# Kernel tuning notes

Measured on AMD Instinct MI355X. Metric: run time of the kernel, lower is better.

## Reference

```python
import jax, jax.numpy as jnp
import numpy as np

E = 1024  # embed_dim

def setup_inputs() -> dict:
    key = jax.random.key(0)
    ks = jax.random.split(key, 7)
    s = 1.0 / np.sqrt(E)  # torch Linear default init scale (uniform bound)
    x = jax.random.normal(ks[0], (4, 2048, E), dtype=jnp.float32)
    Wq = jax.random.uniform(ks[1], (E, E), jnp.float32, -s, s)
    bq = jax.random.uniform(ks[2], (E,), jnp.float32, -s, s)
    Wk = jax.random.uniform(ks[3], (E, E), jnp.float32, -s, s)
    bk = jax.random.uniform(ks[4], (E,), jnp.float32, -s, s)
    Wv = jax.random.uniform(ks[5], (E, E), jnp.float32, -s, s)
    bv = jax.random.uniform(ks[6], (E,), jnp.float32, -s, s)
    return {"x": x, "Wq": Wq, "bq": bq, "Wk": Wk, "bk": bk, "Wv": Wv, "bv": bv}

def reference(x, Wq, bq, Wk, bk, Wv, bv):
    # torch nn.Linear: y = x @ W.T + b
    Q = jnp.einsum('bse,fe->bsf', x, Wq) + bq
    K = jnp.einsum('bse,fe->bsf', x, Wk) + bk
    V = jnp.einsum('bse,fe->bsf', x, Wv) + bv
    scale = jnp.sqrt(jnp.asarray(E, x.dtype))
    scores = jnp.einsum('bqd,bkd->bqk', Q, K) / scale  # [B,S,S]
    attn = jax.nn.softmax(scores, axis=-1)
    return jnp.einsum('bqk,bkd->bqd', attn, V)
```

## Files before the change

### kernel.cpp

```cpp
#include <hip/hip_runtime.h>
#include <hip/hip_bf16.h>


typedef __attribute__((ext_vector_type(8))) short bf16x8;
typedef __attribute__((ext_vector_type(4))) float f32x4;

#define DEVI static __device__ __forceinline__

DEVI short to_bf16(float f) {
    unsigned u = __builtin_bit_cast(unsigned, f);
    u += 0x7fffu + ((u >> 16) & 1u);
    return (short)(u >> 16);
}
DEVI float from_bf16(short s) {
    return __builtin_bit_cast(float, (unsigned)((unsigned short)s) << 16);
}

DEVI void gload_lds16(const short* g, short* l) {
    __builtin_amdgcn_global_load_lds(
        (const __attribute__((address_space(1))) void*)g,
        (__attribute__((address_space(3))) void*)l, 16, 0, 0);
}

template<int BIAS, typename TOUT>
__global__ __launch_bounds__(256, 3)
void gemm97(const short* __restrict__ A, long lda, long bsA,
            const short* __restrict__ B, long ldb, long bsB,
            const float* __restrict__ b0, const float* __restrict__ b1,
            const float* __restrict__ b2,
            TOUT* __restrict__ c0, TOUT* __restrict__ c1, TOUT* __restrict__ c2,
            long ldc, long bsC, int K, float scale)
{
    __shared__ __align__(16) short As[128 * 64];
    __shared__ __align__(16) short Bs[128 * 64];

    const int tid = threadIdx.x;
    const int z = blockIdx.z;

    const int gx = gridDim.x;
    const int nwg = gx * gridDim.y;
    const int id = blockIdx.y * gx + blockIdx.x;
    const int id2 = (id & 7) * (nwg >> 3) + (id >> 3);
    const long m0 = (long)(id2 / gx) * 128;
    const long n0 = (long)(id2 % gx) * 128;

    const short* Ab = A + (long)z * bsA + m0 * lda;
    const short* Bb = B + (long)z * bsB + n0 * ldb;

    const int wv = tid >> 6;
    const int lane = tid & 63;
    const int wr = (wv >> 1) * 64;
    const int wc = (wv & 1) * 64;
    const int lrow = lane & 15;
    const int q = lane >> 4;

    const int NT = K >> 6;

    auto stage = [&](int t) {
        const long k0 = (long)t * 64;
        #pragma unroll
        for (int i = 0; i < 4; ++i) {
            int s = i * 256 + tid;
            int row = s >> 3;
            int src = (s & 7) ^ (row & 7);
            gload_lds16(Ab + (long)row * lda + k0 + src * 8, &As[s * 8]);
        }
        #pragma unroll
        for (int i = 0; i < 4; ++i) {
            int s = i * 256 + tid;
            int row = s >> 3;
            int src = (s & 7) ^ (row & 7);
            gload_lds16(Bb + (long)row * ldb + k0 + src * 8, &Bs[s * 8]);
        }
    };

    f32x4 acc[4][4] = {};

    for (int t = 0; t < NT; ++t) {
        if (t) {
            asm volatile("s_waitcnt lgkmcnt(0)" ::: "memory");
            __builtin_amdgcn_sched_barrier(0);
            __builtin_amdgcn_s_barrier();
        }
        stage(t);
        asm volatile("s_waitcnt vmcnt(0)" ::: "memory");
        __builtin_amdgcn_sched_barrier(0);
        __builtin_amdgcn_s_barrier();

        bf16x8 af[4][2], bf[4][2];
        #pragma unroll
        for (int m = 0; m < 4; ++m) {
            int row = wr + m * 16 + lrow;
            #pragma unroll
            for (int kk = 0; kk < 2; ++kk) {
                int ch = (kk * 4 + q) ^ (row & 7);
                af[m][kk] = *(const bf16x8*)&As[row * 64 + ch * 8];
            }
        }
        #pragma unroll
        for (int n = 0; n < 4; ++n) {
            int row = wc + n * 16 + lrow;
            #pragma unroll
            for (int kk = 0; kk < 2; ++kk) {
                int ch = (kk * 4 + q) ^ (row & 7);
                bf[n][kk] = *(const bf16x8*)&Bs[row * 64 + ch * 8];
            }
        }

        __builtin_amdgcn_s_setprio(1);
        #pragma unroll
        for (int m = 0; m < 4; ++m)
            #pragma unroll
            for (int n = 0; n < 4; ++n)
                #pragma unroll
                for (int kk = 0; kk < 2; ++kk)
                    acc[m][n] = __builtin_amdgcn_mfma_f32_16x16x32_bf16(
                        af[m][kk], bf[n][kk], acc[m][n], 0, 0, 0);
        __builtin_amdgcn_s_setprio(0);
    }

    const float* bias = (BIAS == 2) ? b0
                      : ((z == 0) ? b0 : (z == 1) ? b1 : b2);
    TOUT* Cz = ((z == 0) ? c0 : (z == 1) ? c1 : c2) + (long)z * bsC;
    TOUT* Cb = Cz + m0 * ldc + n0;
    #pragma unroll
    for (int m = 0; m < 4; ++m) {
        #pragma unroll
        for (int n = 0; n < 4; ++n) {
            #pragma unroll
            for (int r = 0; r < 4; ++r) {
                int row = wr + m * 16 + q * 4 + r;
                int col = wc + n * 16 + lrow;
                float v = acc[m][n][r] * scale;
                if constexpr (BIAS == 1) v += bias[n0 + col];
                if constexpr (BIAS == 2) v += bias[m0 + row];
                if constexpr (sizeof(TOUT) == 2)
                    Cb[(long)row * ldc + col] = to_bf16(v);
                else
                    Cb[(long)row * ldc + col] = v;
            }
        }
    }
}

__global__ __launch_bounds__(256)
void cvt_f32_bf16(const float* __restrict__ src, short* __restrict__ dst, int n8)
{
    int i = blockIdx.x * 256 + threadIdx.x;
    if (i < n8) {
        float4 a = ((const float4*)src)[2 * i];
        float4 b = ((const float4*)src)[2 * i + 1];
        bf16x8 o = { to_bf16(a.x), to_bf16(a.y), to_bf16(a.z), to_bf16(a.w),
                     to_bf16(b.x), to_bf16(b.y), to_bf16(b.z), to_bf16(b.w) };
        *(bf16x8*)&dst[i * 8] = o;
    }
}

__global__ __launch_bounds__(256)
void cvt3_f32_bf16(const float* __restrict__ s0, const float* __restrict__ s1,
                   const float* __restrict__ s2, short* __restrict__ dst, int n8)
{
    int zz = blockIdx.y;
    const float* src = (zz == 0) ? s0 : (zz == 1) ? s1 : s2;
    int i = blockIdx.x * 256 + threadIdx.x;
    if (i < n8) {
        float4 a = ((const float4*)src)[2 * i];
        float4 b = ((const float4*)src)[2 * i + 1];
        bf16x8 o = { to_bf16(a.x), to_bf16(a.y), to_bf16(a.z), to_bf16(a.w),
                     to_bf16(b.x), to_bf16(b.y), to_bf16(b.z), to_bf16(b.w) };
        *(bf16x8*)&dst[(long)zz * n8 * 8 + i * 8] = o;
    }
}

__global__ __launch_bounds__(256)
void softmax_rows(short* __restrict__ S, int ncols)
{
    const long row = blockIdx.x;
    short* p = S + row * (long)ncols;
    const int t = threadIdx.x;

    union { bf16x8 v; short s[8]; } u;
    u.v = *(const bf16x8*)&p[t * 8];
    float f[8];
    float m = -3.0e38f;
    #pragma unroll
    for (int j = 0; j < 8; ++j) { f[j] = from_bf16(u.s[j]); m = fmaxf(m, f[j]); }
    #pragma unroll
    for (int off = 32; off > 0; off >>= 1) m = fmaxf(m, __shfl_xor(m, off));

    __shared__ float red[8];
    const int wave = t >> 6;
    if ((t & 63) == 0) red[wave] = m;
    __syncthreads();
    m = fmaxf(fmaxf(red[0], red[1]), fmaxf(red[2], red[3]));

    float sum = 0.f;
    #pragma unroll
    for (int j = 0; j < 8; ++j) { f[j] = __expf(f[j] - m); sum += f[j]; }
    #pragma unroll
    for (int off = 32; off > 0; off >>= 1) sum += __shfl_xor(sum, off);
    if ((t & 63) == 0) red[4 + wave] = sum;
    __syncthreads();
    sum = red[4] + red[5] + red[6] + red[7];

    const float inv = 1.0f / sum;
    #pragma unroll
    for (int j = 0; j < 8; ++j) u.s[j] = to_bf16(f[j] * inv);
    *(bf16x8*)&p[t * 8] = u.v;
}

extern "C" void kernel_launch(void* const* d_in, const int* in_sizes, int n_in,
                              void* d_out, int out_size, void* d_ws, size_t ws_size,
                              hipStream_t stream)
{
    (void)in_sizes; (void)n_in; (void)out_size; (void)ws_size;

    const float* x  = (const float*)d_in[0];
    const float* Wq = (const float*)d_in[1];
    const float* bq = (const float*)d_in[2];
    const float* Wk = (const float*)d_in[3];
    const float* bk = (const float*)d_in[4];
    const float* Wv = (const float*)d_in[5];
    const float* bv = (const float*)d_in[6];
    float* out = (float*)d_out;

    const int S = 2048, E = 1024;
    const long M1 = 1024l * 1024;

    short* w  = (short*)d_ws;
    short* Q  = w;
    short* Kb = w + 8 * M1;
    short* P  = w + 16 * M1;
    short* VT = w + 8 * M1;

    short* dows = (short*)d_out;
    short* xb = dows;
    short* Wb = dows + 8 * M1;

    dim3 blk(256);

    cvt_f32_bf16<<<dim3(4096), blk, 0, stream>>>(x, xb, (int)M1);
    cvt3_f32_bf16<<<dim3(512, 3), blk, 0, stream>>>(Wq, Wk, Wv, Wb, (int)(M1 / 8));

    gemm97<1, short><<<dim3(8, 64, 2), blk, 0, stream>>>(
        xb, E, 0, Wb, E, M1, bq, bk, nullptr, Q, Kb, nullptr, E, 0, E, 1.0f);

    gemm97<0, short><<<dim3(16, 16, 4), blk, 0, stream>>>(
        Q, E, 2 * M1, Kb, E, 2 * M1, nullptr, nullptr, nullptr,
        P, P, P, S, 4 * M1, E, 0.03125f);

    gemm97<2, short><<<dim3(16, 8, 4), blk, 0, stream>>>(
        Wb + 2 * M1, E, 0, xb, E, 2 * M1, bv, nullptr, nullptr,
        VT, VT, VT, S, 2 * M1, E, 1.0f);

    softmax_rows<<<dim3(4 * S), blk, 0, stream>>>(P, S);

    gemm97<0, float><<<dim3(8, 16, 4), blk, 0, stream>>>(
        P, S, 4 * M1, VT, S, 2 * M1, nullptr, nullptr, nullptr,
        out, out, out, E, 2 * M1, S, 1.0f);
}
```

Measured before the change: 188.0 us.

## Fuse exp into QK^T epilogue and deferred normalization into PV epilogue

```diff
diff --git a/kernel.cpp b/kernel.cpp
--- a/kernel.cpp
+++ b/kernel.cpp
@@ -22,14 +22,15 @@
         (__attribute__((address_space(3))) void*)l, 16, 0, 0);
 }
 
-template<int BIAS, typename TOUT>
-__global__ __launch_bounds__(256, 3)
+template<int BIAS, int EPI, typename TOUT>
+__global__ __launch_bounds__(256, 4)
 void gemm97(const short* __restrict__ A, long lda, long bsA,
             const short* __restrict__ B, long ldb, long bsB,
             const float* __restrict__ b0, const float* __restrict__ b1,
             const float* __restrict__ b2,
             TOUT* __restrict__ c0, TOUT* __restrict__ c1, TOUT* __restrict__ c2,
-            long ldc, long bsC, int K, float scale)
+            long ldc, long bsC, int K, float scale,
+            const float* __restrict__ rs, long rsLD)
 {
     __shared__ __align__(16) short As[128 * 64];
     __shared__ __align__(16) short Bs[128 * 64];
@@ -126,14 +127,19 @@
     #pragma unroll
     for (int m = 0; m < 4; ++m) {
         #pragma unroll
-        for (int n = 0; n < 4; ++n) {
-            #pragma unroll
-            for (int r = 0; r < 4; ++r) {
-                int row = wr + m * 16 + q * 4 + r;
+        for (int r = 0; r < 4; ++r) {
+            int row = wr + m * 16 + q * 4 + r;
+            float iv = 1.0f;
+            if constexpr (EPI == 2)
+                iv = 1.0f / rs[(long)z * rsLD + m0 + row];
+            #pragma unroll
+            for (int n = 0; n < 4; ++n) {
                 int col = wc + n * 16 + lrow;
                 float v = acc[m][n][r] * scale;
                 if constexpr (BIAS == 1) v += bias[n0 + col];
                 if constexpr (BIAS == 2) v += bias[m0 + row];
+                if constexpr (EPI == 1) v = __expf(v);
+                if constexpr (EPI == 2) v *= iv;
                 if constexpr (sizeof(TOUT) == 2)
                     Cb[(long)row * ldc + col] = to_bf16(v);
                 else
@@ -173,40 +179,25 @@
 }
 
 __global__ __launch_bounds__(256)
-void softmax_rows(short* __restrict__ S, int ncols)
+void rowsum_rows(const short* __restrict__ S, float* __restrict__ rs, int ncols)
 {
     const long row = blockIdx.x;
-    short* p = S + row * (long)ncols;
+    const short* p = S + row * (long)ncols;
     const int t = threadIdx.x;
 
     union { bf16x8 v; short s[8]; } u;
     u.v = *(const bf16x8*)&p[t * 8];
-    float f[8];
-    float m = -3.0e38f;
-    #pragma unroll
-    for (int j = 0; j < 8; ++j) { f[j] = from_bf16(u.s[j]); m = fmaxf(m, f[j]); }
-    #pragma unroll
-    for (int off = 32; off > 0; off >>= 1) m = fmaxf(m, __shfl_xor(m, off));
-
-    __shared__ float red[8];
-    const int wave = t >> 6;
-    if ((t & 63) == 0) red[wave] = m;
-    __syncthreads();
-    m = fmaxf(fmaxf(red[0], red[1]), fmaxf(red[2], red[3]));
-
     float sum = 0.f;
     #pragma unroll
-    for (int j = 0; j < 8; ++j) { f[j] = __expf(f[j] - m); sum += f[j]; }
+    for (int j = 0; j < 8; ++j) sum += from_bf16(u.s[j]);
     #pragma unroll
     for (int off = 32; off > 0; off >>= 1) sum += __shfl_xor(sum, off);
-    if ((t & 63) == 0) red[4 + wave] = sum;
+
+    __shared__ float red[4];
+    const int wave = t >> 6;
+    if ((t & 63) == 0) red[wave] = sum;
     __syncthreads();
-    sum = red[4] + red[5] + red[6] + red[7];
-
-    const float inv = 1.0f / sum;
-    #pragma unroll
-    for (int j = 0; j < 8; ++j) u.s[j] = to_bf16(f[j] * inv);
-    *(bf16x8*)&p[t * 8] = u.v;
+    if (t == 0) rs[row] = red[0] + red[1] + red[2] + red[3];
 }
 
 extern "C" void kernel_launch(void* const* d_in, const int* in_sizes, int n_in,
@@ -231,6 +222,7 @@
     short* Q  = w;
     short* Kb = w + 8 * M1;
     short* P  = w + 16 * M1;
+    float* rs = (float*)w;
     short* VT = w + 8 * M1;
 
     short* dows = (short*)d_out;
@@ -242,20 +234,21 @@
     cvt_f32_bf16<<<dim3(4096), blk, 0, stream>>>(x, xb, (int)M1);
     cvt3_f32_bf16<<<dim3(512, 3), blk, 0, stream>>>(Wq, Wk, Wv, Wb, (int)(M1 / 8));
 
-    gemm97<1, short><<<dim3(8, 64, 2), blk, 0, stream>>>(
-        xb, E, 0, Wb, E, M1, bq, bk, nullptr, Q, Kb, nullptr, E, 0, E, 1.0f);
-
-    gemm97<0, short><<<dim3(16, 16, 4), blk, 0, stream>>>(
+    gemm97<1, 0, short><<<dim3(8, 64, 2), blk, 0, stream>>>(
+        xb, E, 0, Wb, E, M1, bq, bk, nullptr, Q, Kb, nullptr, E, 0, E, 1.0f,
+        nullptr, 0);
+
+    gemm97<0, 1, short><<<dim3(16, 16, 4), blk, 0, stream>>>(
         Q, E, 2 * M1, Kb, E, 2 * M1, nullptr, nullptr, nullptr,
-        P, P, P, S, 4 * M1, E, 0.03125f);
-
-    gemm97<2, short><<<dim3(16, 8, 4), blk, 0, stream>>>(
+        P, P, P, S, 4 * M1, E, 0.03125f, nullptr, 0);
+
+    gemm97<2, 0, short><<<dim3(16, 8, 4), blk, 0, stream>>>(
         Wb + 2 * M1, E, 0, xb, E, 2 * M1, bv, nullptr, nullptr,
-        VT, VT, VT, S, 2 * M1, E, 1.0f);
-
-    softmax_rows<<<dim3(4 * S), blk, 0, stream>>>(P, S);
-
-    gemm97<0, float><<<dim3(8, 16, 4), blk, 0, stream>>>(
+        VT, VT, VT, S, 2 * M1, E, 1.0f, nullptr, 0);
+
+    rowsum_rows<<<dim3(4 * S), blk, 0, stream>>>(P, rs, S);
+
+    gemm97<0, 2, float><<<dim3(8, 16, 4), blk, 0, stream>>>(
         P, S, 4 * M1, VT, S, 2 * M1, nullptr, nullptr, nullptr,
-        out, out, out, E, 2 * M1, S, 1.0f);
-}
+        out, out, out, E, 2 * M1, S, 1.0f, rs, S);
+}
```

Result: slower. 402.4 us (+114.0%).
